# Kernel tuning notes

Hardware: AMD Instinct MI355X
Metric: run time of the kernel (lower is better)

Reference implementation:

```python
import jax, jax.numpy as jnp
import numpy as np

N_NODES = 714
LRELU = 0.01   # nn.LeakyReLU default
GAT_SLOPE = 0.2  # PyG GATConv internal leaky_relu slope


def _gcn_conv(x, row, col, W, b, n):
    # PyG GCNConv: h = x W; sym-normalized aggregation over edges (self loops already appended)
    h = x @ W
    ones = jnp.ones(row.shape[0], h.dtype)
    deg = jax.ops.segment_sum(ones, col, num_segments=n)
    dinv = jnp.where(deg > 0, jax.lax.rsqrt(deg), 0.0)
    norm = dinv[row] * dinv[col]
    out = jax.ops.segment_sum(h[row] * norm[:, None], col, num_segments=n)
    return out + b


def _gat_conv(x, row, col, W, a_src, a_dst, b, n):
    # PyG GATConv, heads=1: h = x W (no lin bias); edge score = leaky_relu(a_src.h_j + a_dst.h_i)
    h = x @ W
    asrc = h @ a_src
    adst = h @ a_dst
    e = jax.nn.leaky_relu(asrc[row] + adst[col], GAT_SLOPE)
    emax = jax.ops.segment_max(e, col, num_segments=n)
    ee = jnp.exp(e - emax[col])
    denom = jax.ops.segment_sum(ee, col, num_segments=n)
    alpha = ee / (denom[col] + 1e-16)
    out = jax.ops.segment_sum(h[row] * alpha[:, None], col, num_segments=n)
    return out + b


def _forward(feature, edges, poi_tab, cat_tab, lat_tab, long_tab,
             W_in, b_in, gat_W, gat_asrc, gat_adst, gat_b,
             W_out, b_out, W_fc1, b_fc1, W_fc2, b_fc2):
    B, n, _ = feature.shape
    # embedding lookups, concat -> [B, n, 800]
    x = jnp.concatenate([
        poi_tab[feature[..., 0]],
        cat_tab[feature[..., 1]],
        lat_tab[feature[..., 3]],
        long_tab[feature[..., 4]],
    ], axis=-1)
    # append self loops (both GCNConv and GATConv add them by default)
    sl = jnp.arange(n, dtype=edges.dtype)
    sl2 = jnp.broadcast_to(jnp.stack([sl, sl])[None], (B, 2, n))
    ei = jnp.concatenate([edges, sl2], axis=2)  # [B, 2, E+n]
    lrelu = lambda t: jax.nn.leaky_relu(t, LRELU)

    def per_graph(xg, eg):
        row, col = eg[0], eg[1]
        h = lrelu(_gcn_conv(xg, row, col, W_in, b_in, n))
        for i in range(gat_W.shape[0]):  # 3 AGCNUnits, each reuses ONE GATConv twice
            t = _gat_conv(h, row, col, gat_W[i], gat_asrc[i], gat_adst[i], gat_b[i], n)
            h = lrelu(t) + t
            h = lrelu(_gat_conv(h, row, col, gat_W[i], gat_asrc[i], gat_adst[i], gat_b[i], n))
        h = lrelu(_gcn_conv(h, row, col, W_out, b_out, n))  # [n, 1]
        return h[:, 0]

    g = jax.vmap(per_graph)(x, ei)  # [B, n]
    h = jax.nn.leaky_relu(g @ W_fc1 + b_fc1, LRELU)
    return h @ W_fc2 + b_fc2  # [B, 128]


def setup_inputs() -> dict:
    key = jax.random.key(0)
    ks = jax.random.split(key, 20)
    B, E, n = 64, 16384, N_NODES
    C = 128
    feature = jax.random.randint(ks[0], (B, n, 5), 0, 400, dtype=jnp.int64)
    edges = jax.random.randint(ks[1], (B, 2, E), 0, n, dtype=jnp.int64)
    weight = jax.random.normal(ks[2], (B, E, 2), dtype=jnp.float32)
    s = lambda k, shp, fan: (jax.random.normal(k, shp, jnp.float32) / np.sqrt(fan)).astype(jnp.float32)
    return {
        'feature': feature, 'edges': edges, 'weight': weight,
        'poi_tab': s(ks[3], (5099, 300), 1), 'cat_tab': s(ks[4], (400, 100), 1),
        'lat_tab': s(ks[5], (7128, 200), 1), 'long_tab': s(ks[6], (6394, 200), 1),
        'W_in': s(ks[7], (800, C), 800), 'b_in': jnp.zeros((C,), jnp.float32),
        'gat_W': s(ks[8], (3, C, C), C), 'gat_asrc': s(ks[9], (3, C), C),
        'gat_adst': s(ks[10], (3, C), C), 'gat_b': jnp.zeros((3, C), jnp.float32),
        'W_out': s(ks[11], (C, 1), C), 'b_out': jnp.zeros((1,), jnp.float32),
        'W_fc1': s(ks[12], (n, 128), n), 'b_fc1': jnp.zeros((128,), jnp.float32),
        'W_fc2': s(ks[13], (128, 128), 128), 'b_fc2': jnp.zeros((128,), jnp.float32),
    }


def reference(feature, edges, weight, poi_tab, cat_tab, lat_tab, long_tab,
              W_in, b_in, gat_W, gat_asrc, gat_adst, gat_b,
              W_out, b_out, W_fc1, b_fc1, W_fc2, b_fc2):
    # `weight` (edge_attr) is sliced in the original forward but never used in the math
    return _forward(feature, edges, poi_tab, cat_tab, lat_tab, long_tab,
                    W_in, b_in, gat_W, gat_asrc, gat_adst, gat_b,
                    W_out, b_out, W_fc1, b_fc1, W_fc2, b_fc2)
```

## Files before the change

kernel.cpp:

```cpp
#include <hip/hip_runtime.h>


#define BB 64
#define NN 714
#define EE 16384
#define ET (EE + NN)
#define NBt (BB * NN)
#define CC 128
#define RP (NN + 1)
#define DFAST 64
#define KSP 28
#define PROJ_ROWS 19021

typedef _Float16 f16;
typedef __attribute__((ext_vector_type(8))) _Float16 f16x8;
typedef __attribute__((ext_vector_type(4))) _Float16 f16x4;
typedef __attribute__((ext_vector_type(4))) float f32x4;

__device__ __forceinline__ float lrelu01(float x) { return x > 0.f ? x : 0.01f * x; }
__device__ __forceinline__ float lrelu2(float x)  { return x > 0.f ? x : 0.2f  * x; }

__device__ __forceinline__ float wsum(float x) {
#pragma unroll
    for (int o = 32; o > 0; o >>= 1) x += __shfl_xor(x, o);
    return x;
}
__device__ __forceinline__ float qsum(float x) {
#pragma unroll
    for (int o = 8; o > 0; o >>= 1) x += __shfl_xor(x, o);
    return x;
}
__device__ __forceinline__ float qmax(float x) {
#pragma unroll
    for (int o = 8; o > 0; o >>= 1) x = fmaxf(x, __shfl_xor(x, o));
    return x;
}

__device__ __forceinline__ int xcd_swz(int bid, int nwg) {
    int q = nwg >> 3, r = nwg & 7;
    int x = bid & 7, l = bid >> 3;
    int base = (x < r) ? x * (q + 1) : r * (q + 1) + (x - r) * q;
    return base + l;
}

#define NSEG (KSP * 8 * 64)
#define NGAT (3 * 4 * 8 * 64)
#define NPREP (NSEG + NGAT + 3 * CC)
__global__ __launch_bounds__(1024) void k_build_prep(
    const int* __restrict__ edges, int* __restrict__ rowptr,
    int* __restrict__ csr_row, float* __restrict__ dinv,
    const float* __restrict__ W, const float* __restrict__ gat_W,
    const float* __restrict__ a_s, const float* __restrict__ a_d,
    f16* __restrict__ BWh, f16* __restrict__ BWl,
    f16* __restrict__ BGh, f16* __restrict__ BGl,
    float* __restrict__ wsv, float* __restrict__ wdv) {
    __shared__ int degs[NN];
    __shared__ int scan[1024];
    __shared__ int curs[NN];
    int t = threadIdx.x;
    if (blockIdx.x < BB) {
        int b = blockIdx.x;
        if (t < NN) degs[t] = 0;
        __syncthreads();
        int rr[17], cc[17];
#pragma unroll
        for (int q = 0; q < 17; ++q) {
            int e = q * 1024 + t;
            int r = -1, c = -1;
            if (e < ET) {
                if (e < EE) { r = edges[b * 2 * EE + e]; c = edges[b * 2 * EE + EE + e]; }
                else        { r = c = e - EE; }
                atomicAdd(&degs[c], 1);
            }
            rr[q] = r; cc[q] = c;
        }
        __syncthreads();
        int cnt = (t < NN) ? degs[t] : 0;
        scan[t] = cnt;
        __syncthreads();
        for (int off = 1; off < 1024; off <<= 1) {
            int val = (t >= off) ? scan[t - off] : 0;
            __syncthreads();
            scan[t] += val;
            __syncthreads();
        }
        if (t < NN) {
            rowptr[b * RP + t + 1] = scan[t];
            curs[t] = scan[t] - cnt;
            dinv[b * NN + t] = cnt > 0 ? rsqrtf((float)cnt) : 0.f;
        }
        if (t == 0) rowptr[b * RP] = 0;
        __syncthreads();
#pragma unroll
        for (int q = 0; q < 17; ++q) {
            if (cc[q] >= 0) {
                int slot = atomicAdd(&curs[cc[q]], 1);
                csr_row[b * ET + slot] = rr[q];
            }
        }
        return;
    }
    int idx = (blockIdx.x - BB) * 1024 + t;
    if (idx < NSEG) {
        int lane = idx & 63, tc = idx >> 6;
        int ct = tc & 7, ks = tc >> 3;
        int tt = ks < 10 ? 0 : ks < 14 ? 1 : ks < 21 ? 2 : 3;
        int k0 = tt == 0 ? 0 : tt == 1 ? 10 : tt == 2 ? 14 : 21;
        const int Ktab[4] = {300, 100, 200, 200};
        const int Koff[4] = {0, 300, 400, 600};
        int ksl = ks - k0;
        f16x8 ph, pl;
#pragma unroll
        for (int j = 0; j < 8; ++j) {
            int k = ksl * 32 + (lane >> 4) * 8 + j;
            int c = ct * 16 + (lane & 15);
            float v = (k < Ktab[tt]) ? W[(size_t)(Koff[tt] + k) * CC + c] : 0.f;
            f16 hi = (f16)v;
            ph[j] = hi; pl[j] = (f16)(v - (float)hi);
        }
        *(f16x8*)(BWh + (size_t)idx * 8) = ph;
        *(f16x8*)(BWl + (size_t)idx * 8) = pl;
    } else if (idx < NSEG + NGAT) {
        int i2 = idx - NSEG;
        int lane = i2 & 63, tc = i2 >> 6;
        int ct = tc & 7; tc >>= 3;
        int ks = tc & 3, li = tc >> 2;
        const float* Wl = gat_W + (size_t)li * CC * CC;
        f16x8 ph, pl;
#pragma unroll
        for (int j = 0; j < 8; ++j) {
            int k = ks * 32 + (lane >> 4) * 8 + j;
            int c = ct * 16 + (lane & 15);
            float v = Wl[k * CC + c];
            f16 hi = (f16)v;
            ph[j] = hi; pl[j] = (f16)(v - (float)hi);
        }
        *(f16x8*)(BGh + (size_t)i2 * 8) = ph;
        *(f16x8*)(BGl + (size_t)i2 * 8) = pl;
    } else if (idx < NPREP) {
        int i2 = idx - NSEG - NGAT;
        int i = i2 >> 7, k = i2 & 127;
        const float* Wl = gat_W + (size_t)i * CC * CC;
        float s = 0.f, d = 0.f;
#pragma unroll 4
        for (int c = 0; c < CC; ++c) {
            float w = Wl[k * CC + c];
            s = fmaf(w, a_s[i * CC + c], s);
            d = fmaf(w, a_d[i * CC + c], d);
        }
        wsv[i * CC + k] = s; wdv[i * CC + k] = d;
    }
}

__global__ __launch_bounds__(256) void k_proj(
    const float* __restrict__ poi, const float* __restrict__ cat,
    const float* __restrict__ lat, const float* __restrict__ lon,
    const f16* __restrict__ Bh, const f16* __restrict__ Bl,
    float* __restrict__ P) {
    int bid = blockIdx.x;
    int t, r0;
    if (bid < 160)      { t = 0; r0 = bid * 32; }
    else if (bid < 173) { t = 1; r0 = (bid - 160) * 32; }
    else if (bid < 396) { t = 2; r0 = (bid - 173) * 32; }
    else                { t = 3; r0 = (bid - 396) * 32; }
    const int Ktab[4] = {300, 100, 200, 200};
    const int Rtab[4] = {5099, 400, 7128, 6394};
    const int Rofs[4] = {0, 5099, 5499, 12627};
    const int Kst[4]  = {10, 4, 7, 7};
    const int Bks0[4] = {0, 10, 14, 21};
    const float* tab = t == 0 ? poi : t == 1 ? cat : t == 2 ? lat : lon;
    int K = Ktab[t], R = Rtab[t], nks = Kst[t], bks = Bks0[t];
    int lane = threadIdx.x & 63, w = threadIdx.x >> 6;
    int ct0 = w * 2;
    f32x4 acc[2][2];
#pragma unroll
    for (int rt = 0; rt < 2; ++rt)
#pragma unroll
        for (int c = 0; c < 2; ++c) acc[rt][c] = (f32x4){0.f, 0.f, 0.f, 0.f};

    for (int ks = 0; ks < nks; ++ks) {
        int kbase = ks * 32 + (lane >> 4) * 8;
        f16x8 ah[2], al[2];
#pragma unroll
        for (int rt = 0; rt < 2; ++rt) {
            int row = r0 + rt * 16 + (lane & 15);
            int rowc = row < R ? row : R - 1;
            const float* rp = tab + (size_t)rowc * K;
            float v[8];
            if (kbase + 8 <= K) {
                float4 x0 = ((const float4*)(rp + kbase))[0];
                float4 x1 = ((const float4*)(rp + kbase))[1];
                v[0] = x0.x; v[1] = x0.y; v[2] = x0.z; v[3] = x0.w;
                v[4] = x1.x; v[5] = x1.y; v[6] = x1.z; v[7] = x1.w;
            } else if (kbase >= K) {
#pragma unroll
                for (int m = 0; m < 8; ++m) v[m] = 0.f;
            } else {
#pragma unroll
                for (int m = 0; m < 8; ++m) v[m] = (kbase + m < K) ? rp[kbase + m] : 0.f;
            }
#pragma unroll
            for (int j = 0; j < 8; ++j) {
                f16 hi = (f16)v[j];
                ah[rt][j] = hi; al[rt][j] = (f16)(v[j] - (float)hi);
            }
        }
#pragma unroll
        for (int cti = 0; cti < 2; ++cti) {
            int ct = ct0 + cti;
            f16x8 bh = *(const f16x8*)(Bh + ((size_t)((bks + ks) * 8 + ct) * 64 + lane) * 8);
            f16x8 bl = *(const f16x8*)(Bl + ((size_t)((bks + ks) * 8 + ct) * 64 + lane) * 8);
#pragma unroll
            for (int rt = 0; rt < 2; ++rt) {
                acc[rt][cti] = __builtin_amdgcn_mfma_f32_16x16x32_f16(ah[rt], bh, acc[rt][cti], 0, 0, 0);
                acc[rt][cti] = __builtin_amdgcn_mfma_f32_16x16x32_f16(al[rt], bh, acc[rt][cti], 0, 0, 0);
                acc[rt][cti] = __builtin_amdgcn_mfma_f32_16x16x32_f16(ah[rt], bl, acc[rt][cti], 0, 0, 0);
            }
        }
    }
#pragma unroll
    for (int rt = 0; rt < 2; ++rt)
#pragma unroll
        for (int cti = 0; cti < 2; ++cti)
#pragma unroll
            for (int i = 0; i < 4; ++i) {
                int row = r0 + rt * 16 + (lane >> 4) * 4 + i;
                if (row < R) {
                    int col = (ct0 + cti) * 16 + (lane & 15);
                    P[(size_t)(Rofs[t] + row) * CC + col] = acc[rt][cti][i];
                }
            }
}

__global__ __launch_bounds__(256) void k_assemble(
    const int* __restrict__ feature, const float* __restrict__ P,
    f16* __restrict__ out) {
    int tid = xcd_swz(blockIdx.x, gridDim.x) * 256 + threadIdx.x;
    int g = tid >> 4, c8 = (tid & 15) * 8;
    const int* f = feature + (size_t)g * 5;
    const float4* p0 = (const float4*)(P + (size_t)f[0] * CC + c8);
    const float4* p1 = (const float4*)(P + (size_t)(5099 + f[1]) * CC + c8);
    const float4* p2 = (const float4*)(P + (size_t)(5499 + f[3]) * CC + c8);
    const float4* p3 = (const float4*)(P + (size_t)(12627 + f[4]) * CC + c8);
    float4 a0 = p0[0], a1 = p0[1];
    float4 b0 = p1[0], b1 = p1[1];
    float4 c0 = p2[0], c1 = p2[1];
    float4 d0 = p3[0], d1 = p3[1];
    f16x8 r;
    r[0] = (f16)(a0.x + b0.x + c0.x + d0.x);
    r[1] = (f16)(a0.y + b0.y + c0.y + d0.y);
    r[2] = (f16)(a0.z + b0.z + c0.z + d0.z);
    r[3] = (f16)(a0.w + b0.w + c0.w + d0.w);
    r[4] = (f16)(a1.x + b1.x + c1.x + d1.x);
    r[5] = (f16)(a1.y + b1.y + c1.y + d1.y);
    r[6] = (f16)(a1.z + b1.z + c1.z + d1.z);
    r[7] = (f16)(a1.w + b1.w + c1.w + d1.w);
    *(f16x8*)(out + (size_t)g * CC + c8) = r;
}

__global__ __launch_bounds__(256) void k_gat_gemm(
    const f16* __restrict__ hin, const f16* __restrict__ Bh, const f16* __restrict__ Bl,
    const float* __restrict__ wsv, const float* __restrict__ wdv,
    f16* __restrict__ Hp, float* __restrict__ asrc, float* __restrict__ adst) {
    __shared__ __align__(16) f16 Ah[32 * 128];
    __shared__ float reds[256], redd[256];
    int t = threadIdx.x;
    int g0 = xcd_swz(blockIdx.x, gridDim.x) * 32;
    int lane = t & 63, w = t >> 6;
    int sr = t >> 3, skb = (t & 7) * 16;
    const f16x8* hrow = (const f16x8*)(hin + (size_t)(g0 + sr) * CC + skb);
    f16x8 hv0 = hrow[0], hv1 = hrow[1];
    float ps = 0.f, pd = 0.f;
#pragma unroll
    for (int m = 0; m < 8; ++m) {
        ps = fmaf((float)hv0[m], wsv[skb + m], ps);
        pd = fmaf((float)hv0[m], wdv[skb + m], pd);
        ps = fmaf((float)hv1[m], wsv[skb + 8 + m], ps);
        pd = fmaf((float)hv1[m], wdv[skb + 8 + m], pd);
    }
    {
        int kg0 = (t & 7) * 2;
        int ad0 = sr * 128 + ((kg0 ^ (sr & 7)) << 3);
        int ad1 = sr * 128 + (((kg0 + 1) ^ (sr & 7)) << 3);
        *(f16x8*)&Ah[ad0] = hv0;
        *(f16x8*)&Ah[ad1] = hv1;
    }
    reds[t] = ps; redd[t] = pd;
    __syncthreads();
    if (t < 32) {
        float s = 0.f, d = 0.f;
#pragma unroll
        for (int q = 0; q < 8; ++q) { s += reds[t * 8 + q]; d += redd[t * 8 + q]; }
        asrc[g0 + t] = s; adst[g0 + t] = d;
    }
    f32x4 acc[2][2];
#pragma unroll
    for (int rt = 0; rt < 2; ++rt)
#pragma unroll
        for (int c = 0; c < 2; ++c) acc[rt][c] = (f32x4){0.f, 0.f, 0.f, 0.f};
    int ct0 = w * 2;
#pragma unroll
    for (int ks = 0; ks < 4; ++ks) {
        f16x8 ahf[2];
#pragma unroll
        for (int rt = 0; rt < 2; ++rt) {
            int r = rt * 16 + (lane & 15);
            int kg = (lane >> 4) + ks * 4;
            int ad = r * 128 + ((kg ^ (r & 7)) << 3);
            ahf[rt] = *(const f16x8*)&Ah[ad];
        }
#pragma unroll
        for (int cti = 0; cti < 2; ++cti) {
            int ct = ct0 + cti;
            f16x8 bh = *(const f16x8*)(Bh + ((size_t)(ks * 8 + ct) * 64 + lane) * 8);
            f16x8 bl = *(const f16x8*)(Bl + ((size_t)(ks * 8 + ct) * 64 + lane) * 8);
#pragma unroll
            for (int rt = 0; rt < 2; ++rt) {
                acc[rt][cti] = __builtin_amdgcn_mfma_f32_16x16x32_f16(ahf[rt], bh, acc[rt][cti], 0, 0, 0);
                acc[rt][cti] = __builtin_amdgcn_mfma_f32_16x16x32_f16(ahf[rt], bl, acc[rt][cti], 0, 0, 0);
            }
        }
    }
#pragma unroll
    for (int rt = 0; rt < 2; ++rt)
#pragma unroll
        for (int cti = 0; cti < 2; ++cti)
#pragma unroll
            for (int i = 0; i < 4; ++i) {
                int row = g0 + rt * 16 + (lane >> 4) * 4 + i;
                int col = (ct0 + cti) * 16 + (lane & 15);
                Hp[(size_t)row * CC + col] = (f16)acc[rt][cti][i];
            }
}

template <int MODE>
__global__ __launch_bounds__(256) void k_agg(
    const f16* __restrict__ Hp, const float* __restrict__ aux,
    const float* __restrict__ adst, const int* __restrict__ rowptr,
    const int* __restrict__ csr_row, const float* __restrict__ bias,
    f16* __restrict__ out, const float* __restrict__ Wout, float* __restrict__ pscal) {
    __shared__ float2 pr[4][4][DFAST + 2];
    int wid = threadIdx.x >> 6, lane = threadIdx.x & 63;
    int quarter = lane >> 4, ql = lane & 15;
    int g = xcd_swz(blockIdx.x, gridDim.x) * 16 + wid * 4 + quarter;
    int b = g / NN, v = g - b * NN;
    int bN = b * NN, bE = b * ET;
    int s0 = rowptr[b * RP + v], s1 = rowptr[b * RP + v + 1];
    int deg = s1 - s0;

    if (deg <= DFAST) {
        int degp = (deg + 3) & ~3;
        float inv = 1.f;
        int rv[4];
        float wv[4];
        if (MODE == 2) {
            float dv = aux[g];
#pragma unroll
            for (int u = 0; u < 4; ++u) {
                int jj = ql + u * 16;
                rv[u] = 0; wv[u] = 0.f;
                if (jj < deg) { rv[u] = csr_row[bE + s0 + jj]; wv[u] = aux[bN + rv[u]] * dv; }
            }
        } else {
            float adv = adst[g];
            float ev[4];
#pragma unroll
            for (int u = 0; u < 4; ++u) {
                int jj = ql + u * 16;
                rv[u] = 0; ev[u] = -3.0e38f;
                if (jj < deg) { rv[u] = csr_row[bE + s0 + jj]; ev[u] = lrelu2(aux[bN + rv[u]] + adv); }
            }
            float m = qmax(fmaxf(fmaxf(ev[0], ev[1]), fmaxf(ev[2], ev[3])));
            float ss = 0.f;
#pragma unroll
            for (int u = 0; u < 4; ++u) {
                wv[u] = __expf(ev[u] - m);
                ss += wv[u];
            }
            ss = qsum(ss);
            inv = 1.f / (ss + 1e-16f);
        }
#pragma unroll
        for (int u = 0; u < 4; ++u) {
            int jj = ql + u * 16;
            if (jj < degp) pr[wid][quarter][jj] = make_float2(wv[u], __int_as_float(rv[u]));
        }
        const f16* Hb = Hp + (size_t)bN * CC;
        float acc0[8], acc1[8], acc2[8], acc3[8];
#pragma unroll
        for (int j = 0; j < 8; ++j) { acc0[j] = 0.f; acc1[j] = 0.f; acc2[j] = 0.f; acc3[j] = 0.f; }
        for (int jj = 0; jj < degp; jj += 4) {
            float2 p0 = pr[wid][quarter][jj];
            float2 p1 = pr[wid][quarter][jj + 1];
            float2 p2 = pr[wid][quarter][jj + 2];
            float2 p3 = pr[wid][quarter][jj + 3];
            f16x8 h0 = *(const f16x8*)(Hb + (size_t)__float_as_int(p0.y) * CC + ql * 8);
            f16x8 h1 = *(const f16x8*)(Hb + (size_t)__float_as_int(p1.y) * CC + ql * 8);
            f16x8 h2 = *(const f16x8*)(Hb + (size_t)__float_as_int(p2.y) * CC + ql * 8);
            f16x8 h3 = *(const f16x8*)(Hb + (size_t)__float_as_int(p3.y) * CC + ql * 8);
#pragma unroll
            for (int j = 0; j < 8; ++j) {
                acc0[j] = fmaf((float)h0[j], p0.x, acc0[j]);
                acc1[j] = fmaf((float)h1[j], p1.x, acc1[j]);
                acc2[j] = fmaf((float)h2[j], p2.x, acc2[j]);
                acc3[j] = fmaf((float)h3[j], p3.x, acc3[j]);
            }
        }
        float sc = (MODE == 2) ? 1.f : inv;
        float4 bb0 = ((const float4*)bias)[ql * 2];
        float4 bb1 = ((const float4*)bias)[ql * 2 + 1];
        float tv[8], ov[8];
#pragma unroll
        for (int j = 0; j < 8; ++j) {
            float x = acc0[j] + acc1[j] + acc2[j] + acc3[j];
            float bv = (j < 4) ? ((const float*)&bb0)[j] : ((const float*)&bb1)[j - 4];
            tv[j] = x * sc + bv;
            float l = lrelu01(tv[j]);
            ov[j] = (MODE == 0) ? l + tv[j] : l;
        }
        if (MODE == 3) {
            float4 w0v = ((const float4*)Wout)[ql * 2];
            float4 w1v = ((const float4*)Wout)[ql * 2 + 1];
            float p = ov[0] * w0v.x + ov[1] * w0v.y + ov[2] * w0v.z + ov[3] * w0v.w
                    + ov[4] * w1v.x + ov[5] * w1v.y + ov[6] * w1v.z + ov[7] * w1v.w;
            p = qsum(p);
            if (ql == 0) pscal[g] = p;
        } else {
            f16x8 r;
#pragma unroll
            for (int j = 0; j < 8; ++j) r[j] = (f16)ov[j];
            *(f16x8*)(out + (size_t)g * CC + ql * 8) = r;
        }
        return;
    }
    {
        float wsc0 = 0.f;
        float m = 0.f, inv = 1.f, adv = 0.f;
        if (MODE != 2) {
            adv = adst[g];
            m = -3.0e38f;
            for (int j = s0 + ql; j < s1; j += 16)
                m = fmaxf(m, lrelu2(aux[bN + csr_row[bE + j]] + adv));
            m = qmax(m);
            float ssum = 0.f;
            for (int j = s0 + ql; j < s1; j += 16)
                ssum += __expf(lrelu2(aux[bN + csr_row[bE + j]] + adv) - m);
            ssum = qsum(ssum);
            inv = 1.f / (ssum + 1e-16f);
        } else {
            wsc0 = aux[g];
        }
        float acc[8];
#pragma unroll
        for (int j = 0; j < 8; ++j) acc[j] = 0.f;
        for (int j = s0; j < s1; ++j) {
            int r = csr_row[bE + j];
            float wj = (MODE == 2) ? aux[bN + r]
                                   : __expf(lrelu2(aux[bN + r] + adv) - m) * inv;
            f16x8 h = *(const f16x8*)(Hp + (size_t)(bN + r) * CC + ql * 8);
#pragma unroll
            for (int k = 0; k < 8; ++k) acc[k] = fmaf(wj, (float)h[k], acc[k]);
        }
        if (MODE == 2) {
#pragma unroll
            for (int k = 0; k < 8; ++k) acc[k] *= wsc0;
        }
        float4 bb0 = ((const float4*)bias)[ql * 2];
        float4 bb1 = ((const float4*)bias)[ql * 2 + 1];
        float ov[8];
#pragma unroll
        for (int j = 0; j < 8; ++j) {
            float bv = (j < 4) ? ((const float*)&bb0)[j] : ((const float*)&bb1)[j - 4];
            float tvj = acc[j] + bv;
            float l = lrelu01(tvj);
            ov[j] = (MODE == 0) ? l + tvj : l;
        }
        if (MODE == 3) {
            float4 w0v = ((const float4*)Wout)[ql * 2];
            float4 w1v = ((const float4*)Wout)[ql * 2 + 1];
            float p = ov[0] * w0v.x + ov[1] * w0v.y + ov[2] * w0v.z + ov[3] * w0v.w
                    + ov[4] * w1v.x + ov[5] * w1v.y + ov[6] * w1v.z + ov[7] * w1v.w;
            p = qsum(p);
            if (ql == 0) pscal[g] = p;
        } else {
            f16x8 r;
#pragma unroll
            for (int j = 0; j < 8; ++j) r[j] = (f16)ov[j];
            *(f16x8*)(out + (size_t)g * CC + ql * 8) = r;
        }
    }
}

__global__ __launch_bounds__(256) void k_out_agg(
    const float* __restrict__ p, const float* __restrict__ dinv,
    const int* __restrict__ rowptr, const int* __restrict__ csr_row,
    const float* __restrict__ bout, float* __restrict__ gv) {
    int wid = threadIdx.x >> 6, lane = threadIdx.x & 63;
    int quarter = lane >> 4, ql = lane & 15;
    int g = xcd_swz(blockIdx.x, gridDim.x) * 16 + wid * 4 + quarter;
    int b = g / NN, v = g - b * NN;
    int s0 = rowptr[b * RP + v], s1 = rowptr[b * RP + v + 1];
    float acc = 0.f;
    for (int j = s0 + ql; j < s1; j += 16) {
        int r = csr_row[b * ET + j];
        acc += dinv[b * NN + r] * p[b * NN + r];
    }
    acc = qsum(acc);
    if (ql == 0) gv[g] = lrelu01(acc * dinv[g] + bout[0]);
}

__global__ __launch_bounds__(128) void k_fc(
    const float* __restrict__ gv, const float* __restrict__ W1,
    const float* __restrict__ b1, const float* __restrict__ W2,
    const float* __restrict__ b2, float* __restrict__ outp) {
    __shared__ float gs[NN];
    __shared__ float s1[CC];
    int b = blockIdx.x, tx = threadIdx.x;
    for (int v = tx; v < NN; v += 128) gs[v] = gv[b * NN + v];
    __syncthreads();
    float acc = 0.f;
    for (int v = 0; v < NN; ++v) acc = fmaf(gs[v], W1[v * CC + tx], acc);
    float t = lrelu01(acc + b1[tx]);
    s1[tx] = t;
    __syncthreads();
    float acc2 = 0.f;
#pragma unroll
    for (int k = 0; k < CC; ++k) acc2 = fmaf(s1[k], W2[k * CC + tx], acc2);
    outp[b * CC + tx] = acc2 + b2[tx];
}

extern "C" void kernel_launch(void* const* d_in, const int* in_sizes, int n_in,
                              void* d_out, int out_size, void* d_ws, size_t ws_size,
                              hipStream_t stream) {
    const int*   feature  = (const int*)d_in[0];
    const int*   edges    = (const int*)d_in[1];
    const float* poi      = (const float*)d_in[3];
    const float* cat      = (const float*)d_in[4];
    const float* lat      = (const float*)d_in[5];
    const float* lon      = (const float*)d_in[6];
    const float* W_in     = (const float*)d_in[7];
    const float* b_in     = (const float*)d_in[8];
    const float* gat_W    = (const float*)d_in[9];
    const float* gat_asrc = (const float*)d_in[10];
    const float* gat_adst = (const float*)d_in[11];
    const float* gat_b    = (const float*)d_in[12];
    const float* W_out    = (const float*)d_in[13];
    const float* b_out    = (const float*)d_in[14];
    const float* W_fc1    = (const float*)d_in[15];
    const float* b_fc1    = (const float*)d_in[16];
    const float* W_fc2    = (const float*)d_in[17];
    const float* b_fc2    = (const float*)d_in[18];
    float* outp = (float*)d_out;

    char* ws = (char*)d_ws;
    size_t off = 0;
    auto take = [&](size_t bytes) -> char* {
        char* pp = ws + off;
        off = (off + bytes + 255) & ~(size_t)255;
        return pp;
    };
    int*   csr    = (int*)take((size_t)BB * ET * 4);
    int*   rowptr = (int*)take((size_t)BB * RP * 4);
    float* dinv   = (float*)take((size_t)NBt * 4);
    float* asrc   = (float*)take((size_t)NBt * 4);
    float* adst   = (float*)take((size_t)NBt * 4);
    float* pscal  = (float*)take((size_t)NBt * 4);
    float* gvec   = (float*)take((size_t)NBt * 4);
    f16*   bufA   = (f16*)take((size_t)NBt * CC * 2);
    f16*   bufB   = (f16*)take((size_t)NBt * CC * 2);
    float* P      = (float*)take((size_t)PROJ_ROWS * CC * 4);
    f16*   BWh    = (f16*)take((size_t)KSP * 8 * 64 * 8 * 2);
    f16*   BWl    = (f16*)take((size_t)KSP * 8 * 64 * 8 * 2);
    f16*   BGh    = (f16*)take((size_t)3 * 4 * 8 * 64 * 8 * 2);
    f16*   BGl    = (f16*)take((size_t)3 * 4 * 8 * 64 * 8 * 2);
    float* wsv    = (float*)take((size_t)3 * CC * 4);
    float* wdv    = (float*)take((size_t)3 * CC * 4);

    const int prep_blocks = (NPREP + 1023) / 1024;
    k_build_prep<<<BB + prep_blocks, 1024, 0, stream>>>(
        edges, rowptr, csr, dinv,
        W_in, gat_W, gat_asrc, gat_adst, BWh, BWl, BGh, BGl, wsv, wdv);

    k_proj<<<596, 256, 0, stream>>>(poi, cat, lat, lon, BWh, BWl, P);
    k_assemble<<<NBt * 16 / 256, 256, 0, stream>>>(feature, P, bufB);
    k_agg<2><<<NBt / 16, 256, 0, stream>>>(bufB, dinv, nullptr, rowptr, csr, b_in,
                                           bufA, nullptr, nullptr);

    for (int i = 0; i < 3; ++i) {
        const f16* bh = BGh + (size_t)i * 4 * 8 * 64 * 8;
        const f16* bl = BGl + (size_t)i * 4 * 8 * 64 * 8;
        const float* ws_i = wsv + (size_t)i * CC;
        const float* wd_i = wdv + (size_t)i * CC;
        const float* gb = gat_b + (size_t)i * CC;
        k_gat_gemm<<<NBt / 32, 256, 0, stream>>>(bufA, bh, bl, ws_i, wd_i, bufB, asrc, adst);
        k_agg<0><<<NBt / 16, 256, 0, stream>>>(bufB, asrc, adst, rowptr, csr, gb,
                                               bufA, nullptr, nullptr);
        k_gat_gemm<<<NBt / 32, 256, 0, stream>>>(bufA, bh, bl, ws_i, wd_i, bufB, asrc, adst);
        if (i < 2) {
            k_agg<1><<<NBt / 16, 256, 0, stream>>>(bufB, asrc, adst, rowptr, csr, gb,
                                                   bufA, nullptr, nullptr);
        } else {
            k_agg<3><<<NBt / 16, 256, 0, stream>>>(bufB, asrc, adst, rowptr, csr, gb,
                                                   bufA, W_out, pscal);
        }
    }

    k_out_agg<<<NBt / 16, 256, 0, stream>>>(pscal, dinv, rowptr, csr, b_out, gvec);
    k_fc<<<BB, 128, 0, stream>>>(gvec, W_fc1, b_fc1, W_fc2, b_fc2, outp);
}
```

Measured before the change: 273.6 us.

## Aggregate each node with 8 lanes of 16 channels instead of 16 lanes

```diff
diff --git a/kernel.cpp b/kernel.cpp
--- a/kernel.cpp
+++ b/kernel.cpp
@@ -30,9 +30,14 @@
     for (int o = 8; o > 0; o >>= 1) x += __shfl_xor(x, o);
     return x;
 }
-__device__ __forceinline__ float qmax(float x) {
-#pragma unroll
-    for (int o = 8; o > 0; o >>= 1) x = fmaxf(x, __shfl_xor(x, o));
+__device__ __forceinline__ float esum(float x) {
+#pragma unroll
+    for (int o = 4; o > 0; o >>= 1) x += __shfl_xor(x, o);
+    return x;
+}
+__device__ __forceinline__ float emax(float x) {
+#pragma unroll
+    for (int o = 4; o > 0; o >>= 1) x = fmaxf(x, __shfl_xor(x, o));
     return x;
 }
 
@@ -339,97 +344,104 @@
     const float* __restrict__ adst, const int* __restrict__ rowptr,
     const int* __restrict__ csr_row, const float* __restrict__ bias,
     f16* __restrict__ out, const float* __restrict__ Wout, float* __restrict__ pscal) {
-    __shared__ float2 pr[4][4][DFAST + 2];
+    __shared__ float2 pr[4][8][DFAST + 2];
     int wid = threadIdx.x >> 6, lane = threadIdx.x & 63;
-    int quarter = lane >> 4, ql = lane & 15;
-    int g = xcd_swz(blockIdx.x, gridDim.x) * 16 + wid * 4 + quarter;
+    int eighth = lane >> 3, el = lane & 7;
+    int g = xcd_swz(blockIdx.x, gridDim.x) * 32 + wid * 8 + eighth;
     int b = g / NN, v = g - b * NN;
     int bN = b * NN, bE = b * ET;
     int s0 = rowptr[b * RP + v], s1 = rowptr[b * RP + v + 1];
     int deg = s1 - s0;
 
     if (deg <= DFAST) {
-        int degp = (deg + 3) & ~3;
+        int degp = (deg + 1) & ~1;
         float inv = 1.f;
-        int rv[4];
-        float wv[4];
         if (MODE == 2) {
             float dv = aux[g];
 #pragma unroll
-            for (int u = 0; u < 4; ++u) {
-                int jj = ql + u * 16;
-                rv[u] = 0; wv[u] = 0.f;
-                if (jj < deg) { rv[u] = csr_row[bE + s0 + jj]; wv[u] = aux[bN + rv[u]] * dv; }
+            for (int u = 0; u < 8; ++u) {
+                int jj = el + u * 8;
+                int r = 0; float w = 0.f;
+                if (jj < deg) { r = csr_row[bE + s0 + jj]; w = aux[bN + r] * dv; }
+                if (jj < degp) pr[wid][eighth][jj] = make_float2(w, __int_as_float(r));
             }
         } else {
             float adv = adst[g];
-            float ev[4];
-#pragma unroll
-            for (int u = 0; u < 4; ++u) {
-                int jj = ql + u * 16;
+            float ev[8];
+            int rv[8];
+#pragma unroll
+            for (int u = 0; u < 8; ++u) {
+                int jj = el + u * 8;
                 rv[u] = 0; ev[u] = -3.0e38f;
                 if (jj < deg) { rv[u] = csr_row[bE + s0 + jj]; ev[u] = lrelu2(aux[bN + rv[u]] + adv); }
             }
-            float m = qmax(fmaxf(fmaxf(ev[0], ev[1]), fmaxf(ev[2], ev[3])));
+            float mloc = ev[0];
+#pragma unroll
+            for (int u = 1; u < 8; ++u) mloc = fmaxf(mloc, ev[u]);
+            float m = emax(mloc);
             float ss = 0.f;
 #pragma unroll
-            for (int u = 0; u < 4; ++u) {
-                wv[u] = __expf(ev[u] - m);
-                ss += wv[u];
-            }
-            ss = qsum(ss);
+            for (int u = 0; u < 8; ++u) {
+                float w = __expf(ev[u] - m);
+                ss += w;
+                int jj = el + u * 8;
+                if (jj < degp) pr[wid][eighth][jj] = make_float2(w, __int_as_float(rv[u]));
+            }
+            ss = esum(ss);
             inv = 1.f / (ss + 1e-16f);
         }
-#pragma unroll
-        for (int u = 0; u < 4; ++u) {
-            int jj = ql + u * 16;
-            if (jj < degp) pr[wid][quarter][jj] = make_float2(wv[u], __int_as_float(rv[u]));
-        }
         const f16* Hb = Hp + (size_t)bN * CC;
-        float acc0[8], acc1[8], acc2[8], acc3[8];
-#pragma unroll
-        for (int j = 0; j < 8; ++j) { acc0[j] = 0.f; acc1[j] = 0.f; acc2[j] = 0.f; acc3[j] = 0.f; }
-        for (int jj = 0; jj < degp; jj += 4) {
-            float2 p0 = pr[wid][quarter][jj];
-            float2 p1 = pr[wid][quarter][jj + 1];
-            float2 p2 = pr[wid][quarter][jj + 2];
-            float2 p3 = pr[wid][quarter][jj + 3];
-            f16x8 h0 = *(const f16x8*)(Hb + (size_t)__float_as_int(p0.y) * CC + ql * 8);
-            f16x8 h1 = *(const f16x8*)(Hb + (size_t)__float_as_int(p1.y) * CC + ql * 8);
-            f16x8 h2 = *(const f16x8*)(Hb + (size_t)__float_as_int(p2.y) * CC + ql * 8);
-            f16x8 h3 = *(const f16x8*)(Hb + (size_t)__float_as_int(p3.y) * CC + ql * 8);
+        float acc[16];
+#pragma unroll
+        for (int j = 0; j < 16; ++j) acc[j] = 0.f;
+        for (int jj = 0; jj < degp; jj += 2) {
+            float2 p0 = pr[wid][eighth][jj];
+            float2 p1 = pr[wid][eighth][jj + 1];
+            const f16* r0p = Hb + (size_t)__float_as_int(p0.y) * CC + el * 16;
+            const f16* r1p = Hb + (size_t)__float_as_int(p1.y) * CC + el * 16;
+            f16x8 a0 = ((const f16x8*)r0p)[0];
+            f16x8 a1 = ((const f16x8*)r0p)[1];
+            f16x8 b0 = ((const f16x8*)r1p)[0];
+            f16x8 b1 = ((const f16x8*)r1p)[1];
 #pragma unroll
             for (int j = 0; j < 8; ++j) {
-                acc0[j] = fmaf((float)h0[j], p0.x, acc0[j]);
-                acc1[j] = fmaf((float)h1[j], p1.x, acc1[j]);
-                acc2[j] = fmaf((float)h2[j], p2.x, acc2[j]);
-                acc3[j] = fmaf((float)h3[j], p3.x, acc3[j]);
+                acc[j]     = fmaf((float)a0[j], p0.x, acc[j]);
+                acc[8 + j] = fmaf((float)a1[j], p0.x, acc[8 + j]);
+                acc[j]     = fmaf((float)b0[j], p1.x, acc[j]);
+                acc[8 + j] = fmaf((float)b1[j], p1.x, acc[8 + j]);
             }
         }
         float sc = (MODE == 2) ? 1.f : inv;
-        float4 bb0 = ((const float4*)bias)[ql * 2];
-        float4 bb1 = ((const float4*)bias)[ql * 2 + 1];
-        float tv[8], ov[8];
-#pragma unroll
-        for (int j = 0; j < 8; ++j) {
-            float x = acc0[j] + acc1[j] + acc2[j] + acc3[j];
-            float bv = (j < 4) ? ((const float*)&bb0)[j] : ((const float*)&bb1)[j - 4];
-            tv[j] = x * sc + bv;
-            float l = lrelu01(tv[j]);
-            ov[j] = (MODE == 0) ? l + tv[j] : l;
+        float ov[16];
+#pragma unroll
+        for (int q = 0; q < 4; ++q) {
+            float4 bb = ((const float4*)bias)[el * 4 + q];
+#pragma unroll
+            for (int k = 0; k < 4; ++k) {
+                int j = q * 4 + k;
+                float tv = acc[j] * sc + ((const float*)&bb)[k];
+                float l = lrelu01(tv);
+                ov[j] = (MODE == 0) ? l + tv : l;
+            }
         }
         if (MODE == 3) {
-            float4 w0v = ((const float4*)Wout)[ql * 2];
-            float4 w1v = ((const float4*)Wout)[ql * 2 + 1];
-            float p = ov[0] * w0v.x + ov[1] * w0v.y + ov[2] * w0v.z + ov[3] * w0v.w
-                    + ov[4] * w1v.x + ov[5] * w1v.y + ov[6] * w1v.z + ov[7] * w1v.w;
-            p = qsum(p);
-            if (ql == 0) pscal[g] = p;
+            float p = 0.f;
+#pragma unroll
+            for (int q = 0; q < 4; ++q) {
+                float4 wv = ((const float4*)Wout)[el * 4 + q];
+#pragma unroll
+                for (int k = 0; k < 4; ++k)
+                    p = fmaf(ov[q * 4 + k], ((const float*)&wv)[k], p);
+            }
+            p = esum(p);
+            if (el == 0) pscal[g] = p;
         } else {
-            f16x8 r;
-#pragma unroll
-            for (int j = 0; j < 8; ++j) r[j] = (f16)ov[j];
-            *(f16x8*)(out + (size_t)g * CC + ql * 8) = r;
+            f16x8 r0, r1;
+#pragma unroll
+            for (int j = 0; j < 8; ++j) { r0[j] = (f16)ov[j]; r1[j] = (f16)ov[8 + j]; }
+            f16* op = out + (size_t)g * CC + el * 16;
+            ((f16x8*)op)[0] = r0;
+            ((f16x8*)op)[1] = r1;
         }
         return;
     }
@@ -439,54 +451,67 @@
         if (MODE != 2) {
             adv = adst[g];
             m = -3.0e38f;
-            for (int j = s0 + ql; j < s1; j += 16)
+            for (int j = s0 + el; j < s1; j += 8)
                 m = fmaxf(m, lrelu2(aux[bN + csr_row[bE + j]] + adv));
-            m = qmax(m);
+            m = emax(m);
             float ssum = 0.f;
-            for (int j = s0 + ql; j < s1; j += 16)
+            for (int j = s0 + el; j < s1; j += 8)
                 ssum += __expf(lrelu2(aux[bN + csr_row[bE + j]] + adv) - m);
-            ssum = qsum(ssum);
+            ssum = esum(ssum);
             inv = 1.f / (ssum + 1e-16f);
         } else {
             wsc0 = aux[g];
         }
-        float acc[8];
-#pragma unroll
-        for (int j = 0; j < 8; ++j) acc[j] = 0.f;
+        float acc[16];
+#pragma unroll
+        for (int j = 0; j < 16; ++j) acc[j] = 0.f;
         for (int j = s0; j < s1; ++j) {
             int r = csr_row[bE + j];
             float wj = (MODE == 2) ? aux[bN + r]
                                    : __expf(lrelu2(aux[bN + r] + adv) - m) * inv;
-            f16x8 h = *(const f16x8*)(Hp + (size_t)(bN + r) * CC + ql * 8);
-#pragma unroll
-            for (int k = 0; k < 8; ++k) acc[k] = fmaf(wj, (float)h[k], acc[k]);
+            const f16* rp = Hp + (size_t)(bN + r) * CC + el * 16;
+            f16x8 h0 = ((const f16x8*)rp)[0];
+            f16x8 h1 = ((const f16x8*)rp)[1];
+#pragma unroll
+            for (int k = 0; k < 8; ++k) {
+                acc[k]     = fmaf(wj, (float)h0[k], acc[k]);
+                acc[8 + k] = fmaf(wj, (float)h1[k], acc[8 + k]);
+            }
         }
         if (MODE == 2) {
 #pragma unroll
-            for (int k = 0; k < 8; ++k) acc[k] *= wsc0;
-        }
-        float4 bb0 = ((const float4*)bias)[ql * 2];
-        float4 bb1 = ((const float4*)bias)[ql * 2 + 1];
-        float ov[8];
-#pragma unroll
-        for (int j = 0; j < 8; ++j) {
-            float bv = (j < 4) ? ((const float*)&bb0)[j] : ((const float*)&bb1)[j - 4];
-            float tvj = acc[j] + bv;
-            float l = lrelu01(tvj);
-            ov[j] = (MODE == 0) ? l + tvj : l;
+            for (int k = 0; k < 16; ++k) acc[k] *= wsc0;
+        }
+        float ov[16];
+#pragma unroll
+        for (int q = 0; q < 4; ++q) {
+            float4 bb = ((const float4*)bias)[el * 4 + q];
+#pragma unroll
+            for (int k = 0; k < 4; ++k) {
+                int j = q * 4 + k;
+                float tv = acc[j] + ((const float*)&bb)[k];
+                float l = lrelu01(tv);
+                ov[j] = (MODE == 0) ? l + tv : l;
+            }
         }
         if (MODE == 3) {
-            float4 w0v = ((const float4*)Wout)[ql * 2];
-            float4 w1v = ((const float4*)Wout)[ql * 2 + 1];
-            float p = ov[0] * w0v.x + ov[1] * w0v.y + ov[2] * w0v.z + ov[3] * w0v.w
-                    + ov[4] * w1v.x + ov[5] * w1v.y + ov[6] * w1v.z + ov[7] * w1v.w;
-            p = qsum(p);
-            if (ql == 0) pscal[g] = p;
+            float p = 0.f;
+#pragma unroll
+            for (int q = 0; q < 4; ++q) {
+                float4 wv = ((const float4*)Wout)[el * 4 + q];
+#pragma unroll
+                for (int k = 0; k < 4; ++k)
+                    p = fmaf(ov[q * 4 + k], ((const float*)&wv)[k], p);
+            }
+            p = esum(p);
+            if (el == 0) pscal[g] = p;
         } else {
-            f16x8 r;
-#pragma unroll
-            for (int j = 0; j < 8; ++j) r[j] = (f16)ov[j];
-            *(f16x8*)(out + (size_t)g * CC + ql * 8) = r;
+            f16x8 r0, r1;
+#pragma unroll
+            for (int j = 0; j < 8; ++j) { r0[j] = (f16)ov[j]; r1[j] = (f16)ov[8 + j]; }
+            f16* op = out + (size_t)g * CC + el * 16;
+            ((f16x8*)op)[0] = r0;
+            ((f16x8*)op)[1] = r1;
         }
     }
 }
@@ -583,7 +608,7 @@
 
     k_proj<<<596, 256, 0, stream>>>(poi, cat, lat, lon, BWh, BWl, P);
     k_assemble<<<NBt * 16 / 256, 256, 0, stream>>>(feature, P, bufB);
-    k_agg<2><<<NBt / 16, 256, 0, stream>>>(bufB, dinv, nullptr, rowptr, csr, b_in,
+    k_agg<2><<<NBt / 32, 256, 0, stream>>>(bufB, dinv, nullptr, rowptr, csr, b_in,
                                            bufA, nullptr, nullptr);
 
     for (int i = 0; i < 3; ++i) {
@@ -593,14 +618,14 @@
         const float* wd_i = wdv + (size_t)i * CC;
         const float* gb = gat_b + (size_t)i * CC;
         k_gat_gemm<<<NBt / 32, 256, 0, stream>>>(bufA, bh, bl, ws_i, wd_i, bufB, asrc, adst);
-        k_agg<0><<<NBt / 16, 256, 0, stream>>>(bufB, asrc, adst, rowptr, csr, gb,
+        k_agg<0><<<NBt / 32, 256, 0, stream>>>(bufB, asrc, adst, rowptr, csr, gb,
                                                bufA, nullptr, nullptr);
         k_gat_gemm<<<NBt / 32, 256, 0, stream>>>(bufA, bh, bl, ws_i, wd_i, bufB, asrc, adst);
         if (i < 2) {
-            k_agg<1><<<NBt / 16, 256, 0, stream>>>(bufB, asrc, adst, rowptr, csr, gb,
+            k_agg<1><<<NBt / 32, 256, 0, stream>>>(bufB, asrc, adst, rowptr, csr, gb,
                                                    bufA, nullptr, nullptr);
         } else {
-            k_agg<3><<<NBt / 16, 256, 0, stream>>>(bufB, asrc, adst, rowptr, csr, gb,
+            k_agg<3><<<NBt / 32, 256, 0, stream>>>(bufB, asrc, adst, rowptr, csr, gb,
                                                    bufA, W_out, pscal);
         }
     }
```

New measurement: 280.5 us. +2.5%, slower.
